# Optimization experiments

Hardware: AMD Instinct MI355X
Metric: run time of the kernel (lower is better)

Reference implementation:

```python
import jax, jax.numpy as jnp
import numpy as np

DECAY = 0.99
EPS = 1e-5
K = 1024  # num_embeddings
D = 64    # embedding_dim


def setup_inputs() -> dict:
    key = jax.random.key(0)
    k1, k2 = jax.random.split(key)
    inputs = jax.random.normal(k1, (64, 64, 32, 32), dtype=jnp.float32)
    weight = jax.random.uniform(k2, (K, D), minval=-1.0 / K, maxval=1.0 / K, dtype=jnp.float32)
    cluster_size = jnp.zeros((K,), dtype=jnp.float32)
    embed_avg = weight.copy()
    return {"inputs": inputs, "weight": weight, "cluster_size": cluster_size, "embed_avg": embed_avg}


def reference(inputs, weight, cluster_size, embed_avg):
    B, _, H, W = inputs.shape
    # faithful to torch: raw memory-order view(-1, D), no channel permute
    flat = inputs.reshape(-1, D)  # (N, D), N = B*H*W
    distances = (jnp.sum(flat * flat, axis=1, keepdims=True)
                 + jnp.sum(weight * weight, axis=1)
                 - 2.0 * flat @ weight.T)
    idx = jnp.argmin(distances, axis=1)  # (N,)
    quantized = weight[idx].reshape(inputs.shape)  # == onehot @ weight, reshaped

    # EMA codebook update (training path)
    counts = jax.ops.segment_sum(jnp.ones(flat.shape[0], dtype=jnp.float32), idx, num_segments=K)
    cs = DECAY * cluster_size + (1.0 - DECAY) * counts
    n = jnp.sum(cs)
    cs = (cs + EPS) / (n + K * EPS) * n
    dw = jax.ops.segment_sum(flat, idx, num_segments=K)  # == onehot^T @ flat
    new_embed_avg = DECAY * embed_avg + (1.0 - DECAY) * dw
    new_weight = new_embed_avg / cs[:, None]

    # straight-through estimator
    quantized_st = inputs + jax.lax.stop_gradient(quantized - inputs)
    indices = idx.reshape(B, H, W)
    return quantized_st, indices, new_weight, cs, new_embed_avg
```

## Files before the change

kernel.cpp:

```cpp
#include <hip/hip_runtime.h>

#define NROWS 65536
#define KC    1024
#define DD    64

#define QOFF  0
#define IOFF  4194304
#define WOFF  4259840
#define CSOFF 4325376
#define EAOFF 4326400

#define WS_CODESQ  0
#define WS_COUNTS  1056
#define WS_RCCNT   2080
#define WS_CURSOR  2096
#define WS_OFFS    3120
#define WS_CSFIN   4144
#define WS_DW      5168
#define WS_WSWZ    70704
#define WS_IDX     137264
#define WS_RCLIST  202800
#define WS_ROWLIST 268336
#define WS_PACKED  333872

#define MARGIN 5e-5f

typedef _Float16 half8 __attribute__((ext_vector_type(8)));
typedef float    floatx4 __attribute__((ext_vector_type(4)));

struct F4 { float x, y, z, w; };
typedef const __attribute__((address_space(4))) F4    c4F4;
typedef const __attribute__((address_space(4))) float c4f;

__device__ __forceinline__ unsigned f2ord(float f) {
    unsigned u = __float_as_uint(f);
    return (u & 0x80000000u) ? ~u : (u | 0x80000000u);
}

__device__ __forceinline__ float rowsq4(const float4* xv) {
    float4 re, ro;
    re.x = __fmul_rn(xv[0].x, xv[0].x); re.y = __fmul_rn(xv[0].y, xv[0].y);
    re.z = __fmul_rn(xv[0].z, xv[0].z); re.w = __fmul_rn(xv[0].w, xv[0].w);
    ro.x = __fmul_rn(xv[1].x, xv[1].x); ro.y = __fmul_rn(xv[1].y, xv[1].y);
    ro.z = __fmul_rn(xv[1].z, xv[1].z); ro.w = __fmul_rn(xv[1].w, xv[1].w);
#pragma unroll
    for (int i = 2; i < 16; i += 2) {
        re.x = __fadd_rn(re.x, __fmul_rn(xv[i].x, xv[i].x));
        re.y = __fadd_rn(re.y, __fmul_rn(xv[i].y, xv[i].y));
        re.z = __fadd_rn(re.z, __fmul_rn(xv[i].z, xv[i].z));
        re.w = __fadd_rn(re.w, __fmul_rn(xv[i].w, xv[i].w));
        ro.x = __fadd_rn(ro.x, __fmul_rn(xv[i + 1].x, xv[i + 1].x));
        ro.y = __fadd_rn(ro.y, __fmul_rn(xv[i + 1].y, xv[i + 1].y));
        ro.z = __fadd_rn(ro.z, __fmul_rn(xv[i + 1].z, xv[i + 1].z));
        ro.w = __fadd_rn(ro.w, __fmul_rn(xv[i + 1].w, xv[i + 1].w));
    }
    return __fadd_rn(__fadd_rn(__fadd_rn(re.x, re.y), __fadd_rn(re.z, re.w)),
                     __fadd_rn(__fadd_rn(ro.x, ro.y), __fadd_rn(ro.z, ro.w)));
}

__global__ void prep_kernel(const float* __restrict__ weight,
                            float* __restrict__ code_sq,
                            _Float16* __restrict__ wswz,
                            float* __restrict__ counts,
                            int* __restrict__ rccnt) {
    int c = blockIdx.x * blockDim.x + threadIdx.x;
    if (c >= KC) return;
    counts[c] = 0.0f;
    if (c == 0) rccnt[0] = 0;
    float4 wv4[16];
    const float4* pw = reinterpret_cast<const float4*>(weight + (size_t)c * DD);
#pragma unroll
    for (int i = 0; i < 16; ++i) wv4[i] = pw[i];
    code_sq[c] = rowsq4(wv4);
    float w64[64];
#pragma unroll
    for (int i = 0; i < 16; ++i) {
        w64[4 * i] = wv4[i].x; w64[4 * i + 1] = wv4[i].y;
        w64[4 * i + 2] = wv4[i].z; w64[4 * i + 3] = wv4[i].w;
    }
    const int t32 = c >> 5;
    const int s16 = (c >> 4) & 1;
    const int cl  = c & 15;
    const size_t base = (size_t)t32 * 4096 + s16 * 2048 + cl * 8;
#pragma unroll
    for (int q = 0; q < 8; ++q) {
        half8 h, l;
#pragma unroll
        for (int j = 0; j < 8; ++j) {
            float s = w64[q * 8 + j] * 1024.0f;
            _Float16 hh = (_Float16)s;
            h[j] = hh;
            l[j] = (_Float16)(s - (float)hh);
        }
        *reinterpret_cast<half8*>(wswz + base + q * 128)        = h;
        *reinterpret_cast<half8*>(wswz + base + 1024 + q * 128) = l;
    }
}

__global__ __launch_bounds__(512, 4) void vq_scan(
    const float* __restrict__ x_in, const float* __restrict__ code_sq,
    const _Float16* __restrict__ wswz,
    float* __restrict__ out, float* __restrict__ counts,
    int* __restrict__ idxbuf, int* __restrict__ rccnt, int* __restrict__ rclist,
    unsigned long long* __restrict__ packed) {

    __shared__ __align__(16) _Float16 lds_b[2][4096];
    __shared__ float lds_csq[KC];
    __shared__ float sm1[8][32], sm2[8][32];
    __shared__ int   si1[8][32];

    const int tid  = threadIdx.x;
    const int lane = tid & 63;
    const int w    = tid >> 6;
    const int wm   = w & 3;
    const int wsel = w >> 2;
    const int l15  = lane & 15;
    const int g    = lane >> 4;

    const int blockRow0 = blockIdx.x * 128;
    const int waveRow0  = blockRow0 + wm * 32;

    if (tid < 512) {
        lds_csq[tid] = code_sq[tid];
        lds_csq[tid + 512] = code_sq[tid + 512];
    }

    half8 ah[4], al[4];
#pragma unroll
    for (int t = 0; t < 2; ++t) {
#pragma unroll
        for (int kh = 0; kh < 2; ++kh) {
            const float4* p4 = reinterpret_cast<const float4*>(
                x_in + (size_t)(waveRow0 + t * 16 + l15) * DD + kh * 32 + g * 8);
            float4 v0 = p4[0], v1 = p4[1];
            float vals[8] = {v0.x, v0.y, v0.z, v0.w, v1.x, v1.y, v1.z, v1.w};
            half8 hh, ll;
#pragma unroll
            for (int j = 0; j < 8; ++j) {
                _Float16 h = (_Float16)vals[j];
                hh[j] = h;
                ll[j] = (_Float16)(vals[j] - (float)h);
            }
            ah[t * 2 + kh] = hh;
            al[t * 2 + kh] = ll;
        }
    }

    reinterpret_cast<float4*>(lds_b[0])[tid] =
        reinterpret_cast<const float4*>(wswz)[tid];
    __syncthreads();

    float m1[2][4], m2[2][4];
    int   i1[2][4];
#pragma unroll
    for (int t = 0; t < 2; ++t)
#pragma unroll
        for (int r = 0; r < 4; ++r) { m1[t][r] = INFINITY; m2[t][r] = INFINITY; i1[t][r] = 0; }

    int cur = 0;
    for (int ct = 0; ct < 32; ++ct) {
        float4 r0;
        if (ct < 31)
            r0 = reinterpret_cast<const float4*>(wswz + (size_t)(ct + 1) * 4096)[tid];

        const _Float16* S = lds_b[cur] + wsel * 2048;
        half8 bh0 = *reinterpret_cast<const half8*>(S + g * 128 + l15 * 8);
        half8 bh1 = *reinterpret_cast<const half8*>(S + 512 + g * 128 + l15 * 8);
        half8 bl0 = *reinterpret_cast<const half8*>(S + 1024 + g * 128 + l15 * 8);
        half8 bl1 = *reinterpret_cast<const half8*>(S + 1536 + g * 128 + l15 * 8);
        const int code = ct * 32 + wsel * 16 + l15;
        const float csq = lds_csq[code];
#pragma unroll
        for (int t = 0; t < 2; ++t) {
            floatx4 c = {0.f, 0.f, 0.f, 0.f};
            c = __builtin_amdgcn_mfma_f32_16x16x32_f16(al[t * 2 + 0], bh0, c, 0, 0, 0);
            c = __builtin_amdgcn_mfma_f32_16x16x32_f16(al[t * 2 + 1], bh1, c, 0, 0, 0);
            c = __builtin_amdgcn_mfma_f32_16x16x32_f16(ah[t * 2 + 0], bl0, c, 0, 0, 0);
            c = __builtin_amdgcn_mfma_f32_16x16x32_f16(ah[t * 2 + 1], bl1, c, 0, 0, 0);
            c = __builtin_amdgcn_mfma_f32_16x16x32_f16(ah[t * 2 + 0], bh0, c, 0, 0, 0);
            c = __builtin_amdgcn_mfma_f32_16x16x32_f16(ah[t * 2 + 1], bh1, c, 0, 0, 0);
#pragma unroll
            for (int r = 0; r < 4; ++r) {
                float s = fmaf(c[r], -0x1p-9f, csq);
                float mo = m1[t][r];
                m2[t][r] = fminf(fmaxf(s, mo), m2[t][r]);
                i1[t][r] = (s < mo) ? code : i1[t][r];
                m1[t][r] = fminf(mo, s);
            }
        }

        if (ct < 31)
            reinterpret_cast<float4*>(lds_b[cur ^ 1])[tid] = r0;
        __syncthreads();
        cur ^= 1;
    }

#pragma unroll
    for (int t = 0; t < 2; ++t)
#pragma unroll
        for (int r = 0; r < 4; ++r)
#pragma unroll
            for (int mk = 1; mk < 16; mk <<= 1) {
                float o1 = __shfl_xor(m1[t][r], mk);
                float o2 = __shfl_xor(m2[t][r], mk);
                int   oi = __shfl_xor(i1[t][r], mk);
                float n2 = fminf(fminf(m2[t][r], o2), fmaxf(m1[t][r], o1));
                bool sel = (o1 < m1[t][r]) || (o1 == m1[t][r] && oi < i1[t][r]);
                m1[t][r] = sel ? o1 : m1[t][r];
                i1[t][r] = sel ? oi : i1[t][r];
                m2[t][r] = n2;
            }

    if (l15 == 0) {
#pragma unroll
        for (int t = 0; t < 2; ++t)
#pragma unroll
            for (int r = 0; r < 4; ++r) {
                int rib = t * 16 + g * 4 + r;
                sm1[w][rib] = m1[t][r];
                sm2[w][rib] = m2[t][r];
                si1[w][rib] = i1[t][r];
            }
    }
    __syncthreads();

    if (tid < 128) {
        int pwm = tid >> 5;
        int rib = tid & 31;
        float bm1 = sm1[pwm][rib], bm2 = sm2[pwm][rib];
        int bi = si1[pwm][rib];
        {
            float v1 = sm1[pwm | 4][rib];
            float v2 = sm2[pwm | 4][rib];
            int   vi = si1[pwm | 4][rib];
            if (v1 < bm1 || (v1 == bm1 && vi < bi)) {
                bm2 = fminf(bm1, v2);
                bm1 = v1; bi = vi;
            } else {
                bm2 = fminf(bm2, v1);
            }
        }
        int grow = blockRow0 + pwm * 32 + rib;
        if (bm2 - bm1 >= MARGIN) {
            idxbuf[grow] = bi;
            out[IOFF + grow] = (float)bi;
            atomicAdd(&counts[bi], 1.0f);
        } else {
            packed[grow] = 0xFFFFFFFFFFFFFFFFull;
            int pos = atomicAdd(rccnt, 1);
            rclist[pos] = grow;
        }
    }
}

__global__ __launch_bounds__(256, 4) void vq_recheck(
    const float* __restrict__ x_in, const float* __restrict__ weight,
    const float* __restrict__ code_sq,
    unsigned long long* __restrict__ packed,
    const int* __restrict__ rccnt, const int* __restrict__ rclist) {

    const int nrc = rccnt[0];
    const int nitems = ((nrc + 63) >> 6) * 16;

    const int tid  = threadIdx.x;
    const int lane = tid & 63;
    const int wvu  = __builtin_amdgcn_readfirstlane(tid >> 6);

    for (int item = blockIdx.x; item < nitems; item += gridDim.x) {
        const int rb     = (item >> 4) * 64;
        const int cchunk = item & 15;
        const bool valid = (rb + lane) < nrc;
        const int  grow  = rclist[valid ? rb + lane : rb];

        float4 xv[16];
        const float4* px = reinterpret_cast<const float4*>(x_in + (size_t)grow * DD);
#pragma unroll
        for (int i = 0; i < 16; ++i) xv[i] = px[i];
        const float rs = rowsq4(xv);

        const int k0 = cchunk * 64 + wvu * 16;
        unsigned long long wa = (unsigned long long)(weight + (size_t)k0 * DD);
        unsigned long long ca = (unsigned long long)(code_sq + k0);
        unsigned wal = __builtin_amdgcn_readfirstlane((unsigned)wa);
        unsigned wah = __builtin_amdgcn_readfirstlane((unsigned)(wa >> 32));
        unsigned cal = __builtin_amdgcn_readfirstlane((unsigned)ca);
        unsigned cah = __builtin_amdgcn_readfirstlane((unsigned)(ca >> 32));
        c4F4* wb4 = (c4F4*)(((unsigned long long)wah << 32) | wal);
        c4f*  cb  = (c4f*)(((unsigned long long)cah << 32) | cal);

        float best = INFINITY;
        int bidx = 0x7fffffff;

#pragma unroll 2
        for (int k = 0; k < 16; ++k) {
            float a0 = 0.f, a1 = 0.f, a2 = 0.f, a3 = 0.f;
#pragma unroll
            for (int i = 0; i < 16; ++i) {
                F4 w4;
                w4.x = wb4[k * 16 + i].x;
                w4.y = wb4[k * 16 + i].y;
                w4.z = wb4[k * 16 + i].z;
                w4.w = wb4[k * 16 + i].w;
                a0 += xv[i].x * w4.x;
                a1 += xv[i].y * w4.y;
                a2 += xv[i].z * w4.z;
                a3 += xv[i].w * w4.w;
            }
            float dot = (a0 + a1) + (a2 + a3);
            float csq = cb[k];
            float dst = __fsub_rn(__fadd_rn(rs, csq), __fmul_rn(2.0f, dot));
            int kg = k0 + k;
            if (dst < best) { best = dst; bidx = kg; }
        }

        if (valid) {
            unsigned long long p =
                ((unsigned long long)f2ord(best) << 32) | (unsigned)bidx;
            atomicMin(&packed[grow], p);
        }
    }
}

__global__ void rc_finalize(const unsigned long long* __restrict__ packed,
                            const int* __restrict__ rccnt,
                            const int* __restrict__ rclist,
                            float* __restrict__ out, float* __restrict__ counts,
                            int* __restrict__ idxbuf) {
    int i = blockIdx.x * blockDim.x + threadIdx.x;
    if (i >= rccnt[0]) return;
    int grow = rclist[i];
    int bidx = (int)(packed[grow] & 0xFFFFFFFFull);
    out[IOFF + grow] = (float)bidx;
    idxbuf[grow] = bidx;
    atomicAdd(&counts[bidx], 1.0f);
}

__global__ void offsets_cs_kernel(const float* __restrict__ counts,
                                  const float* __restrict__ cluster_size,
                                  int* __restrict__ offs, int* __restrict__ cursor,
                                  float* __restrict__ out, float* __restrict__ cs_fin) {
    __shared__ int   sc[1024];
    __shared__ float sb[1024];
    int k = threadIdx.x;
    int c = (int)counts[k];
    float ce = 0.99f * cluster_size[k] + 0.01f * counts[k];
    sc[k] = c;
    sb[k] = ce;
    __syncthreads();
    for (int off = 1; off < 1024; off <<= 1) {
        int v = (k >= off) ? sc[k - off] : 0;
        __syncthreads();
        sc[k] += v;
        __syncthreads();
    }
    offs[k] = sc[k] - c;
    cursor[k] = 0;
    for (int off = 512; off > 0; off >>= 1) {
        if (k < off) sb[k] += sb[k + off];
        __syncthreads();
    }
    float n = sb[0];
    float v = ((ce + 1e-5f) / (n + 0.01024f)) * n;
    out[CSOFF + k] = v;
    cs_fin[k] = v;
}

__global__ void scatter_kernel(const int* __restrict__ idxbuf,
                               const int* __restrict__ offs,
                               int* __restrict__ cursor,
                               int* __restrict__ rowlist) {
    int r = blockIdx.x * blockDim.x + threadIdx.x;
    if (r >= NROWS) return;
    int k = idxbuf[r];
    int pos = atomicAdd(&cursor[k], 1);
    rowlist[offs[k] + pos] = r;
}

__global__ void dw_q_kernel(const float* __restrict__ x_in,
                            const float* __restrict__ weight,
                            const float* __restrict__ counts,
                            const int* __restrict__ offs,
                            const int* __restrict__ rowlist,
                            const float* __restrict__ embed_avg,
                            const float* __restrict__ cs_fin,
                            float* __restrict__ out, float* __restrict__ dw) {
    __shared__ float wsh[64];
    __shared__ float part[4][64];

    const int k    = blockIdx.x;
    const int tid  = threadIdx.x;
    const int lane = tid & 63;
    const int wv   = tid >> 6;

    if (tid < 64) wsh[tid] = weight[(size_t)k * DD + tid];
    __syncthreads();

    const int cnt  = (int)counts[k];
    const int base = offs[k];
    const float wk = wsh[lane];

    float acc = 0.f;
    int i = wv;
    for (; i + 12 < cnt; i += 16) {
        int r0 = rowlist[base + i];
        int r1 = rowlist[base + i + 4];
        int r2 = rowlist[base + i + 8];
        int r3 = rowlist[base + i + 12];
        float x0 = x_in[(size_t)r0 * DD + lane];
        float x1 = x_in[(size_t)r1 * DD + lane];
        float x2 = x_in[(size_t)r2 * DD + lane];
        float x3 = x_in[(size_t)r3 * DD + lane];
        out[QOFF + (size_t)r0 * DD + lane] = __fadd_rn(x0, __fsub_rn(wk, x0));
        out[QOFF + (size_t)r1 * DD + lane] = __fadd_rn(x1, __fsub_rn(wk, x1));
        out[QOFF + (size_t)r2 * DD + lane] = __fadd_rn(x2, __fsub_rn(wk, x2));
        out[QOFF + (size_t)r3 * DD + lane] = __fadd_rn(x3, __fsub_rn(wk, x3));
        acc = __fadd_rn(acc, x0);
        acc = __fadd_rn(acc, x1);
        acc = __fadd_rn(acc, x2);
        acc = __fadd_rn(acc, x3);
    }
    for (; i < cnt; i += 4) {
        int r = rowlist[base + i];
        float xq = x_in[(size_t)r * DD + lane];
        out[QOFF + (size_t)r * DD + lane] = __fadd_rn(xq, __fsub_rn(wk, xq));
        acc = __fadd_rn(acc, xq);
    }
    part[wv][lane] = acc;
    __syncthreads();
    if (tid < 64) {
        float s = __fadd_rn(__fadd_rn(part[0][tid], part[1][tid]),
                            __fadd_rn(part[2][tid], part[3][tid]));
        int e = k * DD + tid;
        dw[e] = s;
        float na = 0.99f * embed_avg[e] + 0.01f * s;
        out[EAOFF + e] = na;
        out[WOFF + e] = na / cs_fin[k];
    }
}

extern "C" void kernel_launch(void* const* d_in, const int* in_sizes, int n_in,
                              void* d_out, int out_size, void* d_ws, size_t ws_size,
                              hipStream_t stream) {
    (void)in_sizes; (void)n_in; (void)out_size; (void)ws_size;
    const float* x       = (const float*)d_in[0];
    const float* weight  = (const float*)d_in[1];
    const float* cluster = (const float*)d_in[2];
    const float* eavg    = (const float*)d_in[3];
    float* out = (float*)d_out;
    float* wsf = (float*)d_ws;

    float*    code_sq = wsf + WS_CODESQ;
    float*    counts  = wsf + WS_COUNTS;
    int*      rccnt   = (int*)(wsf + WS_RCCNT);
    int*      cursor  = (int*)(wsf + WS_CURSOR);
    int*      offs    = (int*)(wsf + WS_OFFS);
    float*    cs_fin  = wsf + WS_CSFIN;
    float*    dwbuf   = wsf + WS_DW;
    _Float16* wswz    = (_Float16*)(wsf + WS_WSWZ);
    int*      idxbuf  = (int*)(wsf + WS_IDX);
    int*      rclist  = (int*)(wsf + WS_RCLIST);
    int*      rowlist = (int*)(wsf + WS_ROWLIST);
    unsigned long long* packed = (unsigned long long*)(wsf + WS_PACKED);

    hipLaunchKernelGGL(prep_kernel, dim3(16), dim3(64), 0, stream,
                       weight, code_sq, wswz, counts, rccnt);
    hipLaunchKernelGGL(vq_scan, dim3(512), dim3(512), 0, stream,
                       x, code_sq, wswz, out, counts, idxbuf, rccnt, rclist,
                       packed);
    hipLaunchKernelGGL(vq_recheck, dim3(2048), dim3(256), 0, stream,
                       x, weight, code_sq, packed, rccnt, rclist);
    hipLaunchKernelGGL(rc_finalize, dim3(256), dim3(256), 0, stream,
                       packed, rccnt, rclist, out, counts, idxbuf);
    hipLaunchKernelGGL(offsets_cs_kernel, dim3(1), dim3(1024), 0, stream,
                       counts, cluster, offs, cursor, out, cs_fin);
    hipLaunchKernelGGL(scatter_kernel, dim3(256), dim3(256), 0, stream,
                       idxbuf, offs, cursor, rowlist);
    hipLaunchKernelGGL(dw_q_kernel, dim3(1024), dim3(256), 0, stream,
                       x, weight, counts, offs, rowlist, eavg, cs_fin, out, dwbuf);
}
```

Measured before the change: 121.4 us.

## Shrink scan blocks, split MFMA accumulators, fuse recheck finalize into offsets kernel

The distance scan kernel now uses 256-thread blocks covering 64 rows each, doubling the grid, with each thread staging two float4 codebook chunks per tile. The six chained MFMAs are split across two independent accumulators to shorten the dependency chain. The recheck finalize kernel is folded into the single-block offsets/cluster-size kernel using an LDS histogram, which removes one launch but serializes the recheck rows onto one block. Codebook tiles are now reloaded by twice as many blocks.

Result: no change. 120.9 us (-0.4%).

```diff
diff --git a/kernel.cpp b/kernel.cpp
--- a/kernel.cpp
+++ b/kernel.cpp
@@ -97,7 +97,7 @@
     }
 }
 
-__global__ __launch_bounds__(512, 4) void vq_scan(
+__global__ __launch_bounds__(256, 4) void vq_scan(
     const float* __restrict__ x_in, const float* __restrict__ code_sq,
     const _Float16* __restrict__ wswz,
     float* __restrict__ out, float* __restrict__ counts,
@@ -106,24 +106,22 @@
 
     __shared__ __align__(16) _Float16 lds_b[2][4096];
     __shared__ float lds_csq[KC];
-    __shared__ float sm1[8][32], sm2[8][32];
-    __shared__ int   si1[8][32];
+    __shared__ float sm1[4][32], sm2[4][32];
+    __shared__ int   si1[4][32];
 
     const int tid  = threadIdx.x;
     const int lane = tid & 63;
     const int w    = tid >> 6;
-    const int wm   = w & 3;
-    const int wsel = w >> 2;
+    const int wm   = w & 1;
+    const int wsel = w >> 1;
     const int l15  = lane & 15;
     const int g    = lane >> 4;
 
-    const int blockRow0 = blockIdx.x * 128;
+    const int blockRow0 = blockIdx.x * 64;
     const int waveRow0  = blockRow0 + wm * 32;
 
-    if (tid < 512) {
-        lds_csq[tid] = code_sq[tid];
-        lds_csq[tid + 512] = code_sq[tid + 512];
-    }
+#pragma unroll
+    for (int i = 0; i < 4; ++i) lds_csq[tid + i * 256] = code_sq[tid + i * 256];
 
     half8 ah[4], al[4];
 #pragma unroll
@@ -146,8 +144,11 @@
         }
     }
 
-    reinterpret_cast<float4*>(lds_b[0])[tid] =
-        reinterpret_cast<const float4*>(wswz)[tid];
+    {
+        const float4* s = reinterpret_cast<const float4*>(wswz);
+        reinterpret_cast<float4*>(lds_b[0])[tid]       = s[tid];
+        reinterpret_cast<float4*>(lds_b[0])[tid + 256] = s[tid + 256];
+    }
     __syncthreads();
 
     float m1[2][4], m2[2][4];
@@ -159,9 +160,12 @@
 
     int cur = 0;
     for (int ct = 0; ct < 32; ++ct) {
-        float4 r0;
-        if (ct < 31)
-            r0 = reinterpret_cast<const float4*>(wswz + (size_t)(ct + 1) * 4096)[tid];
+        float4 r0, r1;
+        if (ct < 31) {
+            const float4* s = reinterpret_cast<const float4*>(wswz + (size_t)(ct + 1) * 4096);
+            r0 = s[tid];
+            r1 = s[tid + 256];
+        }
 
         const _Float16* S = lds_b[cur] + wsel * 2048;
         half8 bh0 = *reinterpret_cast<const half8*>(S + g * 128 + l15 * 8);
@@ -172,16 +176,17 @@
         const float csq = lds_csq[code];
 #pragma unroll
         for (int t = 0; t < 2; ++t) {
-            floatx4 c = {0.f, 0.f, 0.f, 0.f};
-            c = __builtin_amdgcn_mfma_f32_16x16x32_f16(al[t * 2 + 0], bh0, c, 0, 0, 0);
-            c = __builtin_amdgcn_mfma_f32_16x16x32_f16(al[t * 2 + 1], bh1, c, 0, 0, 0);
-            c = __builtin_amdgcn_mfma_f32_16x16x32_f16(ah[t * 2 + 0], bl0, c, 0, 0, 0);
-            c = __builtin_amdgcn_mfma_f32_16x16x32_f16(ah[t * 2 + 1], bl1, c, 0, 0, 0);
-            c = __builtin_amdgcn_mfma_f32_16x16x32_f16(ah[t * 2 + 0], bh0, c, 0, 0, 0);
-            c = __builtin_amdgcn_mfma_f32_16x16x32_f16(ah[t * 2 + 1], bh1, c, 0, 0, 0);
+            floatx4 c1 = {0.f, 0.f, 0.f, 0.f};
+            floatx4 c2 = {0.f, 0.f, 0.f, 0.f};
+            c1 = __builtin_amdgcn_mfma_f32_16x16x32_f16(al[t * 2 + 0], bh0, c1, 0, 0, 0);
+            c2 = __builtin_amdgcn_mfma_f32_16x16x32_f16(al[t * 2 + 1], bh1, c2, 0, 0, 0);
+            c1 = __builtin_amdgcn_mfma_f32_16x16x32_f16(ah[t * 2 + 0], bl0, c1, 0, 0, 0);
+            c2 = __builtin_amdgcn_mfma_f32_16x16x32_f16(ah[t * 2 + 1], bl1, c2, 0, 0, 0);
+            c1 = __builtin_amdgcn_mfma_f32_16x16x32_f16(ah[t * 2 + 0], bh0, c1, 0, 0, 0);
+            c2 = __builtin_amdgcn_mfma_f32_16x16x32_f16(ah[t * 2 + 1], bh1, c2, 0, 0, 0);
 #pragma unroll
             for (int r = 0; r < 4; ++r) {
-                float s = fmaf(c[r], -0x1p-9f, csq);
+                float s = fmaf(c1[r] + c2[r], -0x1p-9f, csq);
                 float mo = m1[t][r];
                 m2[t][r] = fminf(fmaxf(s, mo), m2[t][r]);
                 i1[t][r] = (s < mo) ? code : i1[t][r];
@@ -189,8 +194,10 @@
             }
         }
 
-        if (ct < 31)
-            reinterpret_cast<float4*>(lds_b[cur ^ 1])[tid] = r0;
+        if (ct < 31) {
+            reinterpret_cast<float4*>(lds_b[cur ^ 1])[tid]       = r0;
+            reinterpret_cast<float4*>(lds_b[cur ^ 1])[tid + 256] = r1;
+        }
         __syncthreads();
         cur ^= 1;
     }
@@ -224,15 +231,15 @@
     }
     __syncthreads();
 
-    if (tid < 128) {
+    if (tid < 64) {
         int pwm = tid >> 5;
         int rib = tid & 31;
         float bm1 = sm1[pwm][rib], bm2 = sm2[pwm][rib];
         int bi = si1[pwm][rib];
         {
-            float v1 = sm1[pwm | 4][rib];
-            float v2 = sm2[pwm | 4][rib];
-            int   vi = si1[pwm | 4][rib];
+            float v1 = sm1[pwm + 2][rib];
+            float v2 = sm2[pwm + 2][rib];
+            int   vi = si1[pwm + 2][rib];
             if (v1 < bm1 || (v1 == bm1 && vi < bi)) {
                 bm2 = fminf(bm1, v2);
                 bm1 = v1; bi = vi;
@@ -321,29 +328,32 @@
     }
 }
 
-__global__ void rc_finalize(const unsigned long long* __restrict__ packed,
-                            const int* __restrict__ rccnt,
-                            const int* __restrict__ rclist,
-                            float* __restrict__ out, float* __restrict__ counts,
-                            int* __restrict__ idxbuf) {
-    int i = blockIdx.x * blockDim.x + threadIdx.x;
-    if (i >= rccnt[0]) return;
-    int grow = rclist[i];
-    int bidx = (int)(packed[grow] & 0xFFFFFFFFull);
-    out[IOFF + grow] = (float)bidx;
-    idxbuf[grow] = bidx;
-    atomicAdd(&counts[bidx], 1.0f);
-}
-
-__global__ void offsets_cs_kernel(const float* __restrict__ counts,
-                                  const float* __restrict__ cluster_size,
-                                  int* __restrict__ offs, int* __restrict__ cursor,
-                                  float* __restrict__ out, float* __restrict__ cs_fin) {
+__global__ void rc_offsets_cs(const unsigned long long* __restrict__ packed,
+                              const int* __restrict__ rccnt,
+                              const int* __restrict__ rclist,
+                              const float* __restrict__ cluster_size,
+                              float* __restrict__ out, int* __restrict__ idxbuf,
+                              float* __restrict__ counts,
+                              int* __restrict__ offs, int* __restrict__ cursor,
+                              float* __restrict__ cs_fin) {
+    __shared__ int   hist[1024];
     __shared__ int   sc[1024];
     __shared__ float sb[1024];
     int k = threadIdx.x;
-    int c = (int)counts[k];
-    float ce = 0.99f * cluster_size[k] + 0.01f * counts[k];
+    hist[k] = 0;
+    __syncthreads();
+    const int nrc = rccnt[0];
+    for (int i = k; i < nrc; i += 1024) {
+        int grow = rclist[i];
+        int bidx = (int)(packed[grow] & 0xFFFFFFFFull);
+        out[IOFF + grow] = (float)bidx;
+        idxbuf[grow] = bidx;
+        atomicAdd(&hist[bidx], 1);
+    }
+    __syncthreads();
+    int c = (int)counts[k] + hist[k];
+    counts[k] = (float)c;
+    float ce = 0.99f * cluster_size[k] + 0.01f * (float)c;
     sc[k] = c;
     sb[k] = ce;
     __syncthreads();
@@ -464,15 +474,14 @@
 
     hipLaunchKernelGGL(prep_kernel, dim3(16), dim3(64), 0, stream,
                        weight, code_sq, wswz, counts, rccnt);
-    hipLaunchKernelGGL(vq_scan, dim3(512), dim3(512), 0, stream,
+    hipLaunchKernelGGL(vq_scan, dim3(1024), dim3(256), 0, stream,
                        x, code_sq, wswz, out, counts, idxbuf, rccnt, rclist,
                        packed);
     hipLaunchKernelGGL(vq_recheck, dim3(2048), dim3(256), 0, stream,
                        x, weight, code_sq, packed, rccnt, rclist);
-    hipLaunchKernelGGL(rc_finalize, dim3(256), dim3(256), 0, stream,
-                       packed, rccnt, rclist, out, counts, idxbuf);
-    hipLaunchKernelGGL(offsets_cs_kernel, dim3(1), dim3(1024), 0, stream,
-                       counts, cluster, offs, cursor, out, cs_fin);
+    hipLaunchKernelGGL(rc_offsets_cs, dim3(1), dim3(1024), 0, stream,
+                       packed, rccnt, rclist, cluster, out, idxbuf, counts,
+                       offs, cursor, cs_fin);
     hipLaunchKernelGGL(scatter_kernel, dim3(256), dim3(256), 0, stream,
                        idxbuf, offs, cursor, rowlist);
     hipLaunchKernelGGL(dw_q_kernel, dim3(1024), dim3(256), 0, stream,
```
